# Kernel optimization log

Measured on AMD Instinct MI355X. Metric: run time of the kernel, lower is better.

The kernel has to match this reference:

```python
import jax, jax.numpy as jnp
import numpy as np


def conv1x1(x, W, b):
    # 1x1 Conv2d == per-pixel linear over channels. x: [B,C,H,W], W: [O,C], b: [O]
    return jnp.einsum('oc,bchw->bohw', W, x) + b[None, :, None, None]


def setup_inputs() -> dict:
    key = jax.random.key(0)
    ks = jax.random.split(key, 18)
    B, C, Hd, H, W = 16, 64, 64, 32, 32
    s = 0.05
    f = jax.random.normal
    return {
        'h': f(ks[0], (B, C, H, W), jnp.float32),
        'm': f(ks[1], (B, C, H, W), jnp.float32),
        'Wq': f(ks[2], (Hd, C), jnp.float32) * s,
        'bq': f(ks[3], (Hd,), jnp.float32) * s,
        'Wk': f(ks[4], (Hd, C), jnp.float32) * s,
        'bk': f(ks[5], (Hd,), jnp.float32) * s,
        'Wk2': f(ks[6], (Hd, C), jnp.float32) * s,
        'bk2': f(ks[7], (Hd,), jnp.float32) * s,
        'Wv': f(ks[8], (C, C), jnp.float32) * s,
        'bv': f(ks[9], (C,), jnp.float32) * s,
        'Wv2': f(ks[10], (C, C), jnp.float32) * s,
        'bv2': f(ks[11], (C,), jnp.float32) * s,
        'Wz': f(ks[12], (2 * C, 2 * C), jnp.float32) * s,
        'bz': f(ks[13], (2 * C,), jnp.float32) * s,
        'Wm': f(ks[14], (3 * C, 3 * C), jnp.float32) * s,
        'bm': f(ks[15], (3 * C,), jnp.float32) * s,
    }


def reference(h, m, Wq, bq, Wk, bk, Wk2, bk2, Wv, bv, Wv2, bv2, Wz, bz, Wm, bm):
    B, C, H, W = h.shape
    Hd = Wq.shape[0]
    N = H * W
    # Shared query from h
    Q_h = conv1x1(h, Wq, bq).reshape(B, Hd, N).transpose(0, 2, 1)  # [B,N,Hd]
    # Self-attention branch over h
    K_h = conv1x1(h, Wk, bk).reshape(B, Hd, N)                     # [B,Hd,N]
    A_h = jax.nn.softmax(jnp.einsum('bnd,bdm->bnm', Q_h, K_h), axis=-1)  # [B,N,N]
    V_h = conv1x1(h, Wv, bv).reshape(B, C, N)                      # [B,C,N]
    Z_h = jnp.einsum('bnm,bcm->bcn', A_h, V_h).reshape(B, C, H, W)
    # Cross-attention branch over memory m (same query Q_h)
    K_m = conv1x1(m, Wk2, bk2).reshape(B, Hd, N)
    A_m = jax.nn.softmax(jnp.einsum('bnd,bdm->bnm', Q_h, K_m), axis=-1)
    V_m = conv1x1(m, Wv2, bv2).reshape(B, C, N)
    Z_m = jnp.einsum('bnm,bcm->bcn', A_m, V_m).reshape(B, C, H, W)
    # Fuse and gated memory update
    Z = conv1x1(jnp.concatenate([Z_h, Z_m], axis=1), Wz, bz)       # [B,2C,H,W]
    combined = conv1x1(jnp.concatenate([Z, h], axis=1), Wm, bm)    # [B,3C,H,W]
    mo, mg, mi = combined[:, :C], combined[:, C:2 * C], combined[:, 2 * C:]
    mi = jax.nn.sigmoid(mi)
    new_m = (1 - mi) * m + mi * jnp.tanh(mg)
    new_h = jax.nn.sigmoid(mo) * new_m
    return (new_h, new_m)
```

## Files before the change

kernel.cpp:

```cpp
#include <hip/hip_runtime.h>

typedef unsigned short u16;
typedef unsigned int u32;
typedef __attribute__((ext_vector_type(8))) short bf16x8;
typedef __attribute__((ext_vector_type(4))) short bf16x4;
typedef __attribute__((ext_vector_type(4))) float f32x4;

#define MFMA(a, b, c) __builtin_amdgcn_mfma_f32_16x16x32_bf16((a), (b), (c), 0, 0, 0)
#define MFMA16(a, b, c) __builtin_amdgcn_mfma_f32_16x16x16bf16_1k((a), (b), (c), 0, 0, 0)

static __device__ __forceinline__ u16 f2bf(float x) {
  u32 u = __float_as_uint(x);
  u += 0x7FFFu + ((u >> 16) & 1u);
  return (u16)(u >> 16);
}
static __device__ __forceinline__ u32 packbf_t(float hi, float lo) {
  return __builtin_amdgcn_perm(__float_as_uint(hi), __float_as_uint(lo), 0x07060302u);
}
static __device__ __forceinline__ u32 packbf(float lo, float hi) {
  return (u32)f2bf(lo) | ((u32)f2bf(hi) << 16);
}

#define NBLK 512u

static __device__ __forceinline__ void grid_barrier(u32* bc) {
  __syncthreads();
  if (threadIdx.x == 0) {
    u32 x;
    asm volatile("s_getreg_b32 %0, hwreg(HW_REG_XCC_ID)" : "=s"(x));
    x &= 7u;
    __hip_atomic_fetch_add(bc + 32 * x, 1u, __ATOMIC_RELAXED, __HIP_MEMORY_SCOPE_AGENT);
    u32 s;
    do {
      __builtin_amdgcn_s_sleep(2);
      s = 0;
#pragma unroll
      for (int i = 0; i < 8; ++i)
        s += __hip_atomic_load(bc + 32 * i, __ATOMIC_RELAXED, __HIP_MEMORY_SCOPE_AGENT);
    } while (s < NBLK);
    u32 F = 0;
#pragma unroll
    for (int i = 0; i < 8; ++i)
      F += (__hip_atomic_load(bc + 32 * i, __ATOMIC_RELAXED, __HIP_MEMORY_SCOPE_AGENT) != 0u)
               ? 1u : 0u;
    if (__hip_atomic_fetch_add(bc + 256 + 32 * x, 1u, __ATOMIC_RELAXED,
                               __HIP_MEMORY_SCOPE_AGENT) == 0u) {
      __threadfence();
      __hip_atomic_fetch_add(bc + 512, 1u, __ATOMIC_RELAXED, __HIP_MEMORY_SCOPE_AGENT);
    }
    while (__hip_atomic_load(bc + 512, __ATOMIC_RELAXED, __HIP_MEMORY_SCOPE_AGENT) < F)
      __builtin_amdgcn_s_sleep(2);
  }
  __syncthreads();
}

__global__ __launch_bounds__(256, 2) void fused_kernel(
    const float* __restrict__ h, const float* __restrict__ m_,
    const float* __restrict__ Wq, const float* __restrict__ bq,
    const float* __restrict__ Wk, const float* __restrict__ bk,
    const float* __restrict__ Wk2, const float* __restrict__ bk2,
    const float* __restrict__ Wv, const float* __restrict__ bv,
    const float* __restrict__ Wv2, const float* __restrict__ bv2,
    const float* __restrict__ Wz, const float* __restrict__ bz,
    const float* __restrict__ Wm, const float* __restrict__ bm,
    float* __restrict__ out,
    u16* __restrict__ Qb, u16* __restrict__ Khb, u16* __restrict__ Kmb,
    u16* __restrict__ Vhb, u16* __restrict__ Vmb, u16* __restrict__ hbuf,
    u16* __restrict__ Ztb, u16* __restrict__ W5, u16* __restrict__ Wzb,
    u16* __restrict__ Wmb, float* __restrict__ bmp, u32* __restrict__ bars)
{
  const int tid = threadIdx.x;
  const int bid = blockIdx.x;

  __shared__ __align__(16) u16 smem[18944];

  {
    const int id = bid * 256 + tid;
    if (id < 20480) {
      const int wi = id >> 12, e = id & 4095;
      const float* src = wi == 0 ? Wq : wi == 1 ? Wk : wi == 2 ? Wk2 : wi == 3 ? Wv : Wv2;
      W5[id] = f2bf(src[e]);
    } else if (id < 36864) {
      const int e = id - 20480;
      Wzb[e] = f2bf(Wz[e]);
    } else if (id < 73728) {
      const int e = id - 36864;
      const int p = e / 192, k = e % 192;
      const int hb2 = p / 96, r1 = p % 96, ctl = r1 / 48, r2 = r1 % 48;
      const int g = r2 >> 4, mm = r2 & 15;
      const int o = g * 64 + (hb2 * 2 + ctl) * 16 + mm;
      Wmb[p * 192 + k] = f2bf(Wm[o * 192 + k]);
    } else if (id < 73920) {
      const int p = id - 73728;
      const int hb2 = p / 96, r1 = p % 96, ctl = r1 / 48, r2 = r1 % 48;
      const int g = r2 >> 4, mm = r2 & 15;
      const int o = g * 64 + (hb2 * 2 + ctl) * 16 + mm;
      bmp[p] = bm[o];
    }
  }

  grid_barrier(bars + 0 * 1024);

  {
    const int n0 = (bid & 15) * 64;
    const int b = (bid >> 4) & 15;
    const int z = bid >> 8;
    u16 (*xt)[72] = (u16(*)[72])smem;
    const float* __restrict__ X = z ? m_ : h;

    {
      const int px = tid & 63, c0 = (tid >> 6) * 16;
#pragma unroll
      for (int i = 0; i < 8; ++i) {
        const int c = c0 + 2 * i;
        const float f0 = X[(b * 64 + c) * 1024 + n0 + px];
        const float f1 = X[(b * 64 + c + 1) * 1024 + n0 + px];
        *(u32*)&xt[px][c] = packbf(f0, f1);
      }
    }
    __syncthreads();

    const int lane = tid & 63, w = tid >> 6;
    const int mm = lane & 15, q = lane >> 4;

    const bf16x8 xa0 = *(const bf16x8*)&xt[w * 16 + mm][q * 8];
    const bf16x8 xa1 = *(const bf16x8*)&xt[w * 16 + mm][32 + q * 8];

    auto qk_store = [&](u16* dst, const u16* Wb, const float* bias) {
#pragma unroll
      for (int ot = 0; ot < 4; ++ot) {
        const bf16x8 wb0 = *(const bf16x8*)(Wb + (ot * 16 + mm) * 64 + q * 8);
        const bf16x8 wb1 = *(const bf16x8*)(Wb + (ot * 16 + mm) * 64 + 32 + q * 8);
        const float4 b4 = *(const float4*)(bias + ot * 16 + q * 4);
        f32x4 d = {b4.x, b4.y, b4.z, b4.w};
        d = MFMA(wb0, xa0, d);
        d = MFMA(wb1, xa1, d);
        uint2 val;
        val.x = packbf(d[0], d[1]);
        val.y = packbf(d[2], d[3]);
        *(uint2*)(dst + (b * 1024 + n0 + w * 16 + mm) * 64 + ot * 16 + q * 4) = val;
      }
    };
    auto v_store = [&](u16* dst, const u16* Wb, const float* bias) {
#pragma unroll
      for (int ot = 0; ot < 4; ++ot) {
        const bf16x8 wb0 = *(const bf16x8*)(Wb + (ot * 16 + mm) * 64 + q * 8);
        const bf16x8 wb1 = *(const bf16x8*)(Wb + (ot * 16 + mm) * 64 + 32 + q * 8);
        const float bb = bias[ot * 16 + mm];
        f32x4 d = {bb, bb, bb, bb};
        d = MFMA(xa0, wb0, d);
        d = MFMA(xa1, wb1, d);
        uint2 val;
        val.x = packbf(d[0], d[1]);
        val.y = packbf(d[2], d[3]);
        *(uint2*)(dst + b * 65536 + (bid & 15) * 4096 + (ot * 16 + mm) * 64 +
                  w * 16 + q * 4) = val;
      }
    };

    if (z == 0) {
      qk_store(Qb, W5, bq);
      qk_store(Khb, W5 + 4096, bk);
      v_store(Vhb, W5 + 3 * 4096, bv);
      const int px = tid >> 2, sg = tid & 3;
      u32* dst = (u32*)(hbuf + (b * 1024 + n0 + px) * 64 + sg * 16);
      const u16* srcr = &xt[px][sg * 16];
#pragma unroll
      for (int j = 0; j < 8; ++j) dst[j] = *(const u32*)(srcr + 2 * j);
    } else {
      qk_store(Kmb, W5 + 2 * 4096, bk2);
      v_store(Vmb, W5 + 4 * 4096, bv2);
    }
  }

  grid_barrier(bars + 1 * 1024);

  {
    const int id = bid;
    const int b = id & 15;
    const int br = (id >> 4) & 1;
    const int qh = id >> 5;
    const u16* __restrict__ K = (br ? Kmb : Khb) + b * 65536;
    const u16* __restrict__ V = (br ? Vmb : Vhb) + b * 65536;

    u16* const pool = smem;
    float (*rsw)[64] = (float(*)[64])(smem + 18432);
    u16* const Kl = pool;
    u16* const Vl = pool + 9216;

    const int w = tid >> 6, lane = tid & 63;
    const int mm = lane & 15, q = lane >> 4;
    const int q0 = qh * 64;

    bf16x8 qb0[4], qb1[4];
#pragma unroll
    for (int qt = 0; qt < 4; ++qt) {
      const u16* Qp = Qb + (b * 1024 + q0 + qt * 16 + mm) * 64;
      qb0[qt] = *(const bf16x8*)(Qp + q * 8);
      qb1[qt] = *(const bf16x8*)(Qp + 32 + q * 8);
    }

    f32x4 z[4][4];
#pragma unroll
    for (int qt = 0; qt < 4; ++qt)
#pragma unroll
      for (int ct = 0; ct < 4; ++ct) z[qt][ct] = (f32x4){0.f, 0.f, 0.f, 0.f};
    float rp[4] = {0.f, 0.f, 0.f, 0.f};

    const int so0 = (tid >> 3) * 72 + (tid & 7) * 8;
    const int so1 = so0 + 32 * 72;
    uint4 sk0, sk1, sv0, sv1;
    auto stage_load = [&](int kc) {
      const u16* Ks = K + kc * 4096;
      const u16* Vs = V + kc * 4096;
      sk0 = *(const uint4*)(Ks + tid * 8);
      sk1 = *(const uint4*)(Ks + tid * 8 + 2048);
      sv0 = *(const uint4*)(Vs + tid * 8);
      sv1 = *(const uint4*)(Vs + tid * 8 + 2048);
    };
    auto stage_store = [&](int buf) {
      u16* Kd = Kl + buf * 4608;
      u16* Vd = Vl + buf * 4608;
      *(uint4*)(Kd + so0) = sk0;
      *(uint4*)(Kd + so1) = sk1;
      *(uint4*)(Vd + so0) = sv0;
      *(uint4*)(Vd + so1) = sv1;
    };

    stage_load(0);
    stage_store(0);
    __syncthreads();

    int cur = 0;
#pragma unroll 1
    for (int kc = 0; kc < 16; ++kc) {
      if (kc < 15) stage_load(kc + 1);

      const u16* Kc = Kl + cur * 4608;
      const u16* Vc = Vl + cur * 4608;
      const bf16x8 kf0 = *(const bf16x8*)(Kc + (w * 16 + mm) * 72 + q * 8);
      const bf16x8 kf1 = *(const bf16x8*)(Kc + (w * 16 + mm) * 72 + 32 + q * 8);
      bf16x4 vf[4];
#pragma unroll
      for (int ct = 0; ct < 4; ++ct)
        vf[ct] = *(const bf16x4*)(Vc + (ct * 16 + mm) * 72 + w * 16 + q * 4);

#pragma unroll
      for (int qt = 0; qt < 4; ++qt) {
        f32x4 s = {0.f, 0.f, 0.f, 0.f};
        s = MFMA(kf0, qb0[qt], s);
        s = MFMA(kf1, qb1[qt], s);
        const float e0 = __expf(s[0]), e1 = __expf(s[1]);
        const float e2 = __expf(s[2]), e3 = __expf(s[3]);
        rp[qt] += (e0 + e1) + (e2 + e3);
        union { u32 u[2]; bf16x4 v; } pb;
        pb.u[0] = packbf_t(e1, e0);
        pb.u[1] = packbf_t(e3, e2);
#pragma unroll
        for (int ct = 0; ct < 4; ++ct) z[qt][ct] = MFMA16(vf[ct], pb.v, z[qt][ct]);
      }

      if (kc < 15) stage_store(cur ^ 1);
      __syncthreads();
      cur ^= 1;
    }

    u16* const zcb = pool;
#pragma unroll
    for (int qt = 0; qt < 4; ++qt) {
      float v = rp[qt];
      v += __shfl_xor(v, 16);
      v += __shfl_xor(v, 32);
      if (q == 0) rsw[w][qt * 16 + mm] = v;
#pragma unroll
      for (int ct = 0; ct < 4; ++ct) {
        uint2 val;
        val.x = packbf_t(z[qt][ct][1], z[qt][ct][0]);
        val.y = packbf_t(z[qt][ct][3], z[qt][ct][2]);
        *(uint2*)(zcb + w * 4352 + (qt * 16 + mm) * 68 + ct * 16 + q * 4) = val;
      }
    }
    __syncthreads();

    const int c2 = tid & 31, qr = tid >> 5;
#pragma unroll
    for (int i = 0; i < 8; ++i) {
      const int query = qr + i * 8;
      const float rt = rsw[0][query] + rsw[1][query] + rsw[2][query] + rsw[3][query];
      const float rinv = __builtin_amdgcn_rcpf(rt);
      float vlo = 0.f, vhi = 0.f;
#pragma unroll
      for (int ww = 0; ww < 4; ++ww) {
        const u32 u = *(const u32*)(zcb + ww * 4352 + query * 68 + c2 * 2);
        vlo += __uint_as_float(u << 16);
        vhi += __uint_as_float(u & 0xffff0000u);
      }
      vlo *= rinv;
      vhi *= rinv;
      *(u32*)(Ztb + (b * 1024 + q0 + query) * 128 + br * 64 + c2 * 2) = packbf_t(vhi, vlo);
    }
  }

  grid_barrier(bars + 2 * 1024);

  {
    const int b = bid >> 5, n0 = (bid & 31) * 32;
    u16 (*zp)[136] = (u16(*)[136])smem;
    const int lane = tid & 63, wv = tid >> 6;
    const int mm = lane & 15, q = lane >> 4;
    const int pxt = wv & 1, oh = wv >> 1;

    {
      bf16x8 za[4];
#pragma unroll
      for (int ks = 0; ks < 4; ++ks)
        za[ks] = *(const bf16x8*)(Ztb + (b * 1024 + n0 + pxt * 16 + mm) * 128 +
                                  ks * 32 + q * 8);
#pragma unroll
      for (int ot = 0; ot < 4; ++ot) {
        const int o0 = oh * 64 + ot * 16;
        const float4 b4 = *(const float4*)(bz + o0 + q * 4);
        f32x4 d = {b4.x, b4.y, b4.z, b4.w};
#pragma unroll
        for (int ks = 0; ks < 4; ++ks) {
          const bf16x8 wb = *(const bf16x8*)(Wzb + (o0 + mm) * 128 + ks * 32 + q * 8);
          d = MFMA(wb, za[ks], d);
        }
        uint2 val;
        val.x = packbf(d[0], d[1]);
        val.y = packbf(d[2], d[3]);
        *(uint2*)&zp[pxt * 16 + mm][o0 + q * 4] = val;
      }
    }
    __syncthreads();

    {
      const int hb2 = oh;
      bf16x8 fa[6];
#pragma unroll
      for (int ks = 0; ks < 4; ++ks)
        fa[ks] = *(const bf16x8*)&zp[pxt * 16 + mm][ks * 32 + q * 8];
      {
        const u16* hp = hbuf + (b * 1024 + n0 + pxt * 16 + mm) * 64;
        fa[4] = *(const bf16x8*)(hp + q * 8);
        fa[5] = *(const bf16x8*)(hp + 32 + q * 8);
      }
      f32x4 dd[6];
#pragma unroll
      for (int j = 0; j < 6; ++j) {
        const int p = hb2 * 96 + j * 16 + mm;
        const float bb = bmp[p];
        f32x4 d = {bb, bb, bb, bb};
#pragma unroll
        for (int ks = 0; ks < 6; ++ks) {
          const bf16x8 wb = *(const bf16x8*)(Wmb + p * 192 + ks * 32 + q * 8);
          d = MFMA(fa[ks], wb, d);
        }
        dd[j] = d;
      }
#pragma unroll
      for (int ctl = 0; ctl < 2; ++ctl) {
        const int c = (hb2 * 2 + ctl) * 16 + mm;
        const int px = n0 + pxt * 16 + q * 4;
        const float4 mold = *(const float4*)(m_ + (b * 64 + c) * 1024 + px);
        float4 nh, nm;
#pragma unroll
        for (int r = 0; r < 4; ++r) {
          const float xo = dd[ctl * 3 + 0][r];
          const float xg = dd[ctl * 3 + 1][r];
          const float xi = dd[ctl * 3 + 2][r];
          const float si = __builtin_amdgcn_rcpf(1.f + __expf(-xi));
          const float th = 1.f - 2.f * __builtin_amdgcn_rcpf(__expf(2.f * xg) + 1.f);
          const float so = __builtin_amdgcn_rcpf(1.f + __expf(-xo));
          const float mo = ((const float*)&mold)[r];
          const float nmv = (1.f - si) * mo + si * th;
          ((float*)&nm)[r] = nmv;
          ((float*)&nh)[r] = so * nmv;
        }
        *(float4*)(out + (b * 64 + c) * 1024 + px) = nh;
        *(float4*)(out + 1048576 + (b * 64 + c) * 1024 + px) = nm;
      }
    }
  }
}

extern "C" void kernel_launch(void* const* d_in, const int* in_sizes, int n_in,
                              void* d_out, int out_size, void* d_ws, size_t ws_size,
                              hipStream_t stream) {
  const float* h   = (const float*)d_in[0];
  const float* m   = (const float*)d_in[1];
  const float* Wq  = (const float*)d_in[2];
  const float* bq  = (const float*)d_in[3];
  const float* Wk  = (const float*)d_in[4];
  const float* bk  = (const float*)d_in[5];
  const float* Wk2 = (const float*)d_in[6];
  const float* bk2 = (const float*)d_in[7];
  const float* Wv  = (const float*)d_in[8];
  const float* bv  = (const float*)d_in[9];
  const float* Wv2 = (const float*)d_in[10];
  const float* bv2 = (const float*)d_in[11];
  const float* Wz  = (const float*)d_in[12];
  const float* bz  = (const float*)d_in[13];
  const float* Wm  = (const float*)d_in[14];
  const float* bm  = (const float*)d_in[15];
  float* out = (float*)d_out;

  char* ws = (char*)d_ws;
  const size_t MB = 1024 * 1024;
  u16* Qb   = (u16*)(ws + 0 * MB);
  u16* Khb  = (u16*)(ws + 2 * MB);
  u16* Kmb  = (u16*)(ws + 4 * MB);
  u16* Vhb  = (u16*)(ws + 6 * MB);
  u16* Vmb  = (u16*)(ws + 8 * MB);
  u16* hbuf = (u16*)(ws + 10 * MB);
  u16* Ztb  = (u16*)(ws + 12 * MB);
  u16* W5   = (u16*)(ws + 16 * MB);
  u16* Wzb  = (u16*)(ws + 16 * MB + 40960);
  u16* Wmb  = (u16*)(ws + 16 * MB + 73728);
  float* bmp = (float*)(ws + 16 * MB + 147456);
  u32* bars  = (u32*)(ws + 16 * MB + 149504);

  hipMemsetAsync(bars, 0, 3 * 4096, stream);
  fused_kernel<<<512, 256, 0, stream>>>(h, m, Wq, bq, Wk, bk, Wk2, bk2, Wv, bv,
                                        Wv2, bv2, Wz, bz, Wm, bm, out, Qb, Khb,
                                        Kmb, Vhb, Vmb, hbuf, Ztb, W5, Wzb, Wmb,
                                        bmp, bars);
}
```

Measured before the change: 164.7 us.

## Drop weight-conversion grid barrier and stream K/V straight from global into registers

The Q/K/V projection now reads fp32 weights and converts them to bf16 inline, so the W5 staging buffer and the first grid-wide barrier are gone. The attention loop no longer stages K and V tiles through double-buffered shared memory with __syncthreads. Each wave instead loads its MFMA fragments directly from global memory, with a one-step register prefetch. This removes one grid barrier and the per-chunk block syncs, in exchange for redundant per-wave global loads of K/V that have less coalescing and rely on L2/cache hits.

```diff
diff --git a/kernel.cpp b/kernel.cpp
--- a/kernel.cpp
+++ b/kernel.cpp
@@ -66,7 +66,7 @@
     float* __restrict__ out,
     u16* __restrict__ Qb, u16* __restrict__ Khb, u16* __restrict__ Kmb,
     u16* __restrict__ Vhb, u16* __restrict__ Vmb, u16* __restrict__ hbuf,
-    u16* __restrict__ Ztb, u16* __restrict__ W5, u16* __restrict__ Wzb,
+    u16* __restrict__ Ztb, u16* __restrict__ Wzb,
     u16* __restrict__ Wmb, float* __restrict__ bmp, u32* __restrict__ bars)
 {
   const int tid = threadIdx.x;
@@ -76,21 +76,17 @@
 
   {
     const int id = bid * 256 + tid;
-    if (id < 20480) {
-      const int wi = id >> 12, e = id & 4095;
-      const float* src = wi == 0 ? Wq : wi == 1 ? Wk : wi == 2 ? Wk2 : wi == 3 ? Wv : Wv2;
-      W5[id] = f2bf(src[e]);
-    } else if (id < 36864) {
+    if (id >= 20480 && id < 36864) {
       const int e = id - 20480;
       Wzb[e] = f2bf(Wz[e]);
-    } else if (id < 73728) {
+    } else if (id >= 36864 && id < 73728) {
       const int e = id - 36864;
       const int p = e / 192, k = e % 192;
       const int hb2 = p / 96, r1 = p % 96, ctl = r1 / 48, r2 = r1 % 48;
       const int g = r2 >> 4, mm = r2 & 15;
       const int o = g * 64 + (hb2 * 2 + ctl) * 16 + mm;
       Wmb[p * 192 + k] = f2bf(Wm[o * 192 + k]);
-    } else if (id < 73920) {
+    } else if (id >= 73728 && id < 73920) {
       const int p = id - 73728;
       const int hb2 = p / 96, r1 = p % 96, ctl = r1 / 48, r2 = r1 % 48;
       const int g = r2 >> 4, mm = r2 & 15;
@@ -98,8 +94,6 @@
       bmp[p] = bm[o];
     }
   }
-
-  grid_barrier(bars + 0 * 1024);
 
   {
     const int n0 = (bid & 15) * 64;
@@ -126,11 +120,22 @@
     const bf16x8 xa0 = *(const bf16x8*)&xt[w * 16 + mm][q * 8];
     const bf16x8 xa1 = *(const bf16x8*)&xt[w * 16 + mm][32 + q * 8];
 
-    auto qk_store = [&](u16* dst, const u16* Wb, const float* bias) {
+    auto ldw8 = [&](const float* Wf, int row, int col0) {
+      const float4 a = *(const float4*)(Wf + row * 64 + col0);
+      const float4 bvec = *(const float4*)(Wf + row * 64 + col0 + 4);
+      union { u32 u[4]; bf16x8 v; } r;
+      r.u[0] = packbf(a.x, a.y);
+      r.u[1] = packbf(a.z, a.w);
+      r.u[2] = packbf(bvec.x, bvec.y);
+      r.u[3] = packbf(bvec.z, bvec.w);
+      return r.v;
+    };
+
+    auto qk_store = [&](u16* dst, const float* Wf, const float* bias) {
 #pragma unroll
       for (int ot = 0; ot < 4; ++ot) {
-        const bf16x8 wb0 = *(const bf16x8*)(Wb + (ot * 16 + mm) * 64 + q * 8);
-        const bf16x8 wb1 = *(const bf16x8*)(Wb + (ot * 16 + mm) * 64 + 32 + q * 8);
+        const bf16x8 wb0 = ldw8(Wf, ot * 16 + mm, q * 8);
+        const bf16x8 wb1 = ldw8(Wf, ot * 16 + mm, 32 + q * 8);
         const float4 b4 = *(const float4*)(bias + ot * 16 + q * 4);
         f32x4 d = {b4.x, b4.y, b4.z, b4.w};
         d = MFMA(wb0, xa0, d);
@@ -141,11 +146,11 @@
         *(uint2*)(dst + (b * 1024 + n0 + w * 16 + mm) * 64 + ot * 16 + q * 4) = val;
       }
     };
-    auto v_store = [&](u16* dst, const u16* Wb, const float* bias) {
+    auto v_store = [&](u16* dst, const float* Wf, const float* bias) {
 #pragma unroll
       for (int ot = 0; ot < 4; ++ot) {
-        const bf16x8 wb0 = *(const bf16x8*)(Wb + (ot * 16 + mm) * 64 + q * 8);
-        const bf16x8 wb1 = *(const bf16x8*)(Wb + (ot * 16 + mm) * 64 + 32 + q * 8);
+        const bf16x8 wb0 = ldw8(Wf, ot * 16 + mm, q * 8);
+        const bf16x8 wb1 = ldw8(Wf, ot * 16 + mm, 32 + q * 8);
         const float bb = bias[ot * 16 + mm];
         f32x4 d = {bb, bb, bb, bb};
         d = MFMA(xa0, wb0, d);
@@ -159,34 +164,32 @@
     };
 
     if (z == 0) {
-      qk_store(Qb, W5, bq);
-      qk_store(Khb, W5 + 4096, bk);
-      v_store(Vhb, W5 + 3 * 4096, bv);
+      qk_store(Qb, Wq, bq);
+      qk_store(Khb, Wk, bk);
+      v_store(Vhb, Wv, bv);
       const int px = tid >> 2, sg = tid & 3;
       u32* dst = (u32*)(hbuf + (b * 1024 + n0 + px) * 64 + sg * 16);
       const u16* srcr = &xt[px][sg * 16];
 #pragma unroll
       for (int j = 0; j < 8; ++j) dst[j] = *(const u32*)(srcr + 2 * j);
     } else {
-      qk_store(Kmb, W5 + 2 * 4096, bk2);
-      v_store(Vmb, W5 + 4 * 4096, bv2);
+      qk_store(Kmb, Wk2, bk2);
+      v_store(Vmb, Wv2, bv2);
     }
   }
 
-  grid_barrier(bars + 1 * 1024);
+  grid_barrier(bars + 0 * 1024);
 
   {
     const int id = bid;
     const int b = id & 15;
     const int br = (id >> 4) & 1;
     const int qh = id >> 5;
-    const u16* __restrict__ K = (br ? Kmb : Khb) + b * 65536;
-    const u16* __restrict__ V = (br ? Vmb : Vhb) + b * 65536;
-
-    u16* const pool = smem;
+    const u16* __restrict__ Kg = (br ? Kmb : Khb) + b * 65536;
+    const u16* __restrict__ Vg = (br ? Vmb : Vhb) + b * 65536;
+
+    u16* const zcb = smem;
     float (*rsw)[64] = (float(*)[64])(smem + 18432);
-    u16* const Kl = pool;
-    u16* const Vl = pool + 9216;
 
     const int w = tid >> 6, lane = tid & 63;
     const int mm = lane & 15, q = lane >> 4;
@@ -207,44 +210,12 @@
       for (int ct = 0; ct < 4; ++ct) z[qt][ct] = (f32x4){0.f, 0.f, 0.f, 0.f};
     float rp[4] = {0.f, 0.f, 0.f, 0.f};
 
-    const int so0 = (tid >> 3) * 72 + (tid & 7) * 8;
-    const int so1 = so0 + 32 * 72;
-    uint4 sk0, sk1, sv0, sv1;
-    auto stage_load = [&](int kc) {
-      const u16* Ks = K + kc * 4096;
-      const u16* Vs = V + kc * 4096;
-      sk0 = *(const uint4*)(Ks + tid * 8);
-      sk1 = *(const uint4*)(Ks + tid * 8 + 2048);
-      sv0 = *(const uint4*)(Vs + tid * 8);
-      sv1 = *(const uint4*)(Vs + tid * 8 + 2048);
-    };
-    auto stage_store = [&](int buf) {
-      u16* Kd = Kl + buf * 4608;
-      u16* Vd = Vl + buf * 4608;
-      *(uint4*)(Kd + so0) = sk0;
-      *(uint4*)(Kd + so1) = sk1;
-      *(uint4*)(Vd + so0) = sv0;
-      *(uint4*)(Vd + so1) = sv1;
-    };
-
-    stage_load(0);
-    stage_store(0);
-    __syncthreads();
-
-    int cur = 0;
-#pragma unroll 1
-    for (int kc = 0; kc < 16; ++kc) {
-      if (kc < 15) stage_load(kc + 1);
-
-      const u16* Kc = Kl + cur * 4608;
-      const u16* Vc = Vl + cur * 4608;
-      const bf16x8 kf0 = *(const bf16x8*)(Kc + (w * 16 + mm) * 72 + q * 8);
-      const bf16x8 kf1 = *(const bf16x8*)(Kc + (w * 16 + mm) * 72 + 32 + q * 8);
-      bf16x4 vf[4];
-#pragma unroll
-      for (int ct = 0; ct < 4; ++ct)
-        vf[ct] = *(const bf16x4*)(Vc + (ct * 16 + mm) * 72 + w * 16 + q * 4);
-
+    const int koff = (w * 16 + mm) * 64 + q * 8;
+    const int voff = mm * 64 + w * 16 + q * 4;
+
+    auto attn_step = [&](const bf16x8& kf0, const bf16x8& kf1,
+                         const bf16x4& v0, const bf16x4& v1,
+                         const bf16x4& v2, const bf16x4& v3) {
 #pragma unroll
       for (int qt = 0; qt < 4; ++qt) {
         f32x4 s = {0.f, 0.f, 0.f, 0.f};
@@ -256,16 +227,36 @@
         union { u32 u[2]; bf16x4 v; } pb;
         pb.u[0] = packbf_t(e1, e0);
         pb.u[1] = packbf_t(e3, e2);
-#pragma unroll
-        for (int ct = 0; ct < 4; ++ct) z[qt][ct] = MFMA16(vf[ct], pb.v, z[qt][ct]);
-      }
-
-      if (kc < 15) stage_store(cur ^ 1);
-      __syncthreads();
-      cur ^= 1;
-    }
-
-    u16* const zcb = pool;
+        z[qt][0] = MFMA16(v0, pb.v, z[qt][0]);
+        z[qt][1] = MFMA16(v1, pb.v, z[qt][1]);
+        z[qt][2] = MFMA16(v2, pb.v, z[qt][2]);
+        z[qt][3] = MFMA16(v3, pb.v, z[qt][3]);
+      }
+    };
+
+    bf16x8 ck0 = *(const bf16x8*)(Kg + koff);
+    bf16x8 ck1 = *(const bf16x8*)(Kg + koff + 32);
+    bf16x4 cv0 = *(const bf16x4*)(Vg + voff);
+    bf16x4 cv1 = *(const bf16x4*)(Vg + voff + 1024);
+    bf16x4 cv2 = *(const bf16x4*)(Vg + voff + 2048);
+    bf16x4 cv3 = *(const bf16x4*)(Vg + voff + 3072);
+
+#pragma unroll 1
+    for (int kc = 0; kc < 15; ++kc) {
+      const u16* Kn = Kg + (kc + 1) * 4096;
+      const u16* Vn = Vg + (kc + 1) * 4096;
+      const bf16x8 nk0 = *(const bf16x8*)(Kn + koff);
+      const bf16x8 nk1 = *(const bf16x8*)(Kn + koff + 32);
+      const bf16x4 nv0 = *(const bf16x4*)(Vn + voff);
+      const bf16x4 nv1 = *(const bf16x4*)(Vn + voff + 1024);
+      const bf16x4 nv2 = *(const bf16x4*)(Vn + voff + 2048);
+      const bf16x4 nv3 = *(const bf16x4*)(Vn + voff + 3072);
+      attn_step(ck0, ck1, cv0, cv1, cv2, cv3);
+      ck0 = nk0; ck1 = nk1;
+      cv0 = nv0; cv1 = nv1; cv2 = nv2; cv3 = nv3;
+    }
+    attn_step(ck0, ck1, cv0, cv1, cv2, cv3);
+
 #pragma unroll
     for (int qt = 0; qt < 4; ++qt) {
       float v = rp[qt];
@@ -301,7 +292,7 @@
     }
   }
 
-  grid_barrier(bars + 2 * 1024);
+  grid_barrier(bars + 1 * 1024);
 
   {
     const int b = bid >> 5, n0 = (bid & 31) * 32;
@@ -414,15 +405,14 @@
   u16* Vmb  = (u16*)(ws + 8 * MB);
   u16* hbuf = (u16*)(ws + 10 * MB);
   u16* Ztb  = (u16*)(ws + 12 * MB);
-  u16* W5   = (u16*)(ws + 16 * MB);
   u16* Wzb  = (u16*)(ws + 16 * MB + 40960);
   u16* Wmb  = (u16*)(ws + 16 * MB + 73728);
   float* bmp = (float*)(ws + 16 * MB + 147456);
   u32* bars  = (u32*)(ws + 16 * MB + 149504);
 
-  hipMemsetAsync(bars, 0, 3 * 4096, stream);
+  hipMemsetAsync(bars, 0, 2 * 4096, stream);
   fused_kernel<<<512, 256, 0, stream>>>(h, m, Wq, bq, Wk, bk, Wk2, bk2, Wv, bv,
                                         Wv2, bv2, Wz, bz, Wm, bm, out, Qb, Khb,
-                                        Kmb, Vhb, Vmb, hbuf, Ztb, W5, Wzb, Wmb,
+                                        Kmb, Vhb, Vmb, hbuf, Ztb, Wzb, Wmb,
                                         bmp, bars);
 }
```

After: 164.9 us. About the same (+0.2%).
